# Kernel optimization log

Measured on AMD Instinct MI355X. Metric: run time of the kernel, lower is better.

The kernel has to match this reference:

```python
import jax, jax.numpy as jnp
import numpy as np

N_NODES = 50000
N_EDGES = 1600000
IN_DIM, HIDDEN, OUT_DIM = 128, 128, 64


def setup_inputs() -> dict:
    key = jax.random.key(0)
    ks = jax.random.split(key, 8)
    x = jax.random.normal(ks[0], (N_NODES, IN_DIM), dtype=jnp.float32)
    edge_index = jax.random.randint(ks[1], (2, N_EDGES), 0, N_NODES, dtype=jnp.int64)
    # SAGEConv params: lin_l applied to aggregated neighbors (with bias),
    # lin_r applied to root/self features (no bias) -- PyG defaults.
    def lin_init(k, fan_in, fan_out):
        bound = 1.0 / np.sqrt(fan_in)
        return jax.random.uniform(k, (fan_in, fan_out), jnp.float32, -bound, bound)
    W1_l = lin_init(ks[2], IN_DIM, HIDDEN)
    W1_r = lin_init(ks[3], IN_DIM, HIDDEN)
    b1 = jnp.zeros((HIDDEN,), jnp.float32)
    W2_l = lin_init(ks[4], HIDDEN, OUT_DIM)
    W2_r = lin_init(ks[5], HIDDEN, OUT_DIM)
    b2 = jnp.zeros((OUT_DIM,), jnp.float32)
    return {"x": x, "edge_index": edge_index, "W1_l": W1_l, "W1_r": W1_r,
            "b1": b1, "W2_l": W2_l, "W2_r": W2_r, "b2": b2}


def _sage_conv(h, src, dst, n_nodes, W_l, W_r, b):
    # gather messages from source nodes, mean-aggregate at destinations
    msg = h[src]                                              # [E, D]
    agg_sum = jax.ops.segment_sum(msg, dst, num_segments=n_nodes)
    deg = jax.ops.segment_sum(jnp.ones((src.shape[0],), h.dtype), dst,
                              num_segments=n_nodes)
    agg_mean = agg_sum / jnp.maximum(deg, 1.0)[:, None]       # [N, D]
    return agg_mean @ W_l + h @ W_r + b


def reference(x, edge_index, W1_l, W1_r, b1, W2_l, W2_r, b2):
    n = x.shape[0]
    src, dst = edge_index[0], edge_index[1]
    h = jax.nn.relu(_sage_conv(x, src, dst, n, W1_l, W1_r, b1))
    return _sage_conv(h, src, dst, n, W2_l, W2_r, b2)
```

## Files before the change

kernel.cpp:

```cpp
#include <hip/hip_runtime.h>

#define NN 50000
#define NE 1600000
#define BSTRIDE 96
#define BNODES 25
#define C_BKT 2000
#define P1_BLKS 256
#define P1_CHUNK 6250
#define ZID 50000
#define XCVT_BLKS 1563
#define WCVT_BLKS 48
#define PP_PREP (XCVT_BLKS + WCVT_BLKS)
#define RGRP 3128

typedef __bf16 bf16x8 __attribute__((ext_vector_type(8)));
typedef float  f32x4  __attribute__((ext_vector_type(4)));
typedef float  f32x2  __attribute__((ext_vector_type(2)));

__device__ __forceinline__ float bfLo(uint u) { union { uint i; float f; } v; v.i = u << 16; return v.f; }
__device__ __forceinline__ float bfHi(uint u) { union { uint i; float f; } v; v.i = u & 0xffff0000u; return v.f; }
__device__ __forceinline__ f32x2 bfPair(uint u) {
    union { uint i[2]; f32x2 f; } v; v.i[0] = u << 16; v.i[1] = u & 0xffff0000u; return v.f;
}
__device__ __forceinline__ ushort f2bf(float f) {
    union { float f; uint i; } v; v.f = f;
    uint r = v.i + 0x7fffu + ((v.i >> 16) & 1u);
    return (ushort)(r >> 16);
}
__device__ __forceinline__ uint pack2(float a, float b) {
    return (uint)f2bf(a) | ((uint)f2bf(b) << 16);
}
__device__ __forceinline__ bf16x8 load8(const ushort* p) {
    union { uint4 u; bf16x8 b; } v; v.u = *(const uint4*)p; return v.b;
}

#define ACC8P(u) { b0 += bfPair(u.x); b1 += bfPair(u.y); b2 += bfPair(u.z); b3 += bfPair(u.w); }

#define CVA(u, o) { f32x2 p0 = __builtin_amdgcn_cvt_pk_f32_fp8((int)(u), 0); \
                    f32x2 p1 = __builtin_amdgcn_cvt_pk_f32_fp8((int)(u), 1); \
                    a[(o)] += p0; a[(o)+1] += p1; }
#define ACCF8(v) { CVA((v).x, 0); CVA((v).y, 2); CVA((v).z, 4); CVA((v).w, 6); }

__device__ __forceinline__ int pkOff(int n, int k) {
    return (((n >> 4) * 4 + (k >> 5)) * 512) + (((k >> 3) & 3) * 128) + ((n & 15) * 8) + (k & 7);
}

__global__ __launch_bounds__(1024) void k_pp(
    const float4* __restrict__ x, ushort* __restrict__ xbp, uint* __restrict__ xf8,
    const float* __restrict__ W1l, const float* __restrict__ W1r,
    const float* __restrict__ W2l, const float* __restrict__ W2r,
    ushort* __restrict__ T1l, ushort* __restrict__ T1r,
    ushort* __restrict__ T2l, ushort* __restrict__ T2r,
    const int* __restrict__ src, const int* __restrict__ dst,
    uint* __restrict__ cells, uint* __restrict__ offc, ushort* __restrict__ hW) {
    __shared__ uint hist[C_BKT + 1];
    __shared__ uint part[250];
    const int b = blockIdx.x;
    const int tid = threadIdx.x;
    if (b < XCVT_BLKS) {
        int i = b * 1024 + tid;
        if (i < NN * 128 / 4) {
            float4 v = x[i];
            int r = i >> 5, k0 = (i & 31) * 4;
            ushort4 o; o.x = f2bf(v.x); o.y = f2bf(v.y); o.z = f2bf(v.z); o.w = f2bf(v.w);
            *(ushort4*)(xbp + pkOff(r, k0)) = o;
            uint rr = (uint)__builtin_amdgcn_cvt_pk_fp8_f32(v.x, v.y, 0, 0);
            rr = (uint)__builtin_amdgcn_cvt_pk_fp8_f32(v.z, v.w, (int)rr, 1);
            xf8[i] = rr;
        } else if (b == XCVT_BLKS - 1) {
            if (tid >= 512 && tid < 544) xf8[(size_t)ZID * 32 + (tid - 512)] = 0;
            else if (tid >= 544 && tid < 576) ((uint*)hW)[(size_t)ZID * 32 + (tid - 544)] = 0;
        }
    } else if (b < PP_PREP) {
        int i = (b - XCVT_BLKS) * 1024 + tid;
        if (i < 16384) {
            int k = i >> 7, n = i & 127; T1l[pkOff(n, k)] = f2bf(W1l[i]);
        } else if (i < 32768) {
            int j = i - 16384; int k = j >> 7, n = j & 127; T1r[pkOff(n, k)] = f2bf(W1r[j]);
        } else if (i < 40960) {
            int j = i - 32768; int k = j >> 6, n = j & 63;  T2l[pkOff(n, k)] = f2bf(W2l[j]);
        } else {
            int j = i - 40960; int k = j >> 6, n = j & 63;  T2r[pkOff(n, k)] = f2bf(W2r[j]);
        }
    } else {
        const int b2 = b - PP_PREP;
        for (int i = tid; i < C_BKT; i += 1024) hist[i] = 0;
        __syncthreads();
        const int beg = b2 * P1_CHUNK;
        for (int i = beg + tid; i < beg + P1_CHUNK; i += 1024)
            atomicAdd(&hist[dst[i] / BNODES], 1);
        __syncthreads();
        if (tid < 250) {
            uint s = 0;
            #pragma unroll
            for (int k = 0; k < 8; k++) {
                uint t = hist[tid * 8 + k];
                hist[tid * 8 + k] = s;
                s += t;
            }
            part[tid] = s;
        }
        __syncthreads();
        if (tid == 0) {
            uint run = 0;
            for (int t = 0; t < 250; t++) { uint tmp = part[t]; part[t] = run; run += tmp; }
        }
        __syncthreads();
        if (tid < 250) {
            uint bs = part[tid];
            if (bs) {
                #pragma unroll
                for (int k = 0; k < 8; k++) hist[tid * 8 + k] += bs;
            }
        }
        __syncthreads();
        for (int c = tid; c < C_BKT; c += 1024) {
            uint st = hist[c];
            uint en = (c == C_BKT - 1) ? (uint)P1_CHUNK : hist[c + 1];
            offc[(size_t)c * P1_BLKS + b2] = st | ((en - st) << 16);
        }
        __syncthreads();
        uint* myCells = cells + (size_t)b2 * P1_CHUNK;
        for (int i = beg + tid; i < beg + P1_CHUNK; i += 1024) {
            int d = dst[i];
            int s = src[i];
            int c = d / BNODES;
            uint p = atomicAdd(&hist[c], 1);
            myCells[p] = ((uint)(d - c * BNODES) << 16) | (uint)s;
        }
    }
}

__global__ __launch_bounds__(256) void k_pagg(
    const uint* __restrict__ cells, const uint* __restrict__ offc,
    const uchar* __restrict__ xf8, ushort* __restrict__ col,
    int* __restrict__ deg, ushort* __restrict__ aggp) {
    __shared__ uint hist[BNODES];
    __shared__ __align__(16) ushort colS[BNODES * BSTRIDE];
    const int bid = blockIdx.x;
    const int c = (bid & 7) * 250 + (bid >> 3);
    const int tid = threadIdx.x;
    if (tid < BNODES) hist[tid] = 0;
    __syncthreads();
    {
        uint v = offc[(size_t)c * P1_BLKS + tid];
        int st = (int)(v & 0xFFFF), n = (int)(v >> 16);
        const uint* cell = cells + (size_t)tid * P1_CHUNK + st;
        for (int j = 0; j < n; j++) {
            uint e = cell[j];
            int dl = e >> 16;
            uint p = atomicAdd(&hist[dl], 1);
            if (p < BSTRIDE) colS[dl * BSTRIDE + p] = (ushort)(e & 0xFFFF);
        }
    }
    __syncthreads();
    const int nodeBase = c * BNODES;
    if (tid < BNODES) {
        deg[nodeBase + tid] = (int)hist[tid];
        int dd = min((int)hist[tid], BSTRIDE);
        int dr = (dd + 7) & ~7;
        for (int j = dd; j < dr; j++) colS[tid * BSTRIDE + j] = (ushort)ZID;
    }
    __syncthreads();
    {
        uint4* cg = (uint4*)(col + (size_t)nodeBase * BSTRIDE);
        const uint4* cs = (const uint4*)colS;
        for (int i = tid; i < BNODES * BSTRIDE / 8; i += 256) cg[i] = cs[i];
    }
    const int wave = tid >> 6, lane = tid & 63;
    const int q = lane >> 3;
    const int cc = lane & 7;
    for (int ln = wave; ln < BNODES; ln += 4) {
        int d = (int)hist[ln];
        int dd = min(d, BSTRIDE);
        int nb = ((dd + 7) & ~7) >> 3;
        const int base = ln * BSTRIDE;
        f32x2 a[8];
        #pragma unroll
        for (int i = 0; i < 8; i++) a[i] = (f32x2){0.f, 0.f};
        int t = 0;
        for (; t + 4 <= nb; t += 4) {
            int s0 = (int)colS[base + t * 8 + q];
            int s1 = (int)colS[base + t * 8 + 8 + q];
            int s2 = (int)colS[base + t * 8 + 16 + q];
            int s3 = (int)colS[base + t * 8 + 24 + q];
            uint4 u0 = *(const uint4*)(xf8 + (size_t)s0 * 128 + cc * 16);
            uint4 u1 = *(const uint4*)(xf8 + (size_t)s1 * 128 + cc * 16);
            uint4 u2 = *(const uint4*)(xf8 + (size_t)s2 * 128 + cc * 16);
            uint4 u3 = *(const uint4*)(xf8 + (size_t)s3 * 128 + cc * 16);
            ACCF8(u0); ACCF8(u1); ACCF8(u2); ACCF8(u3);
        }
        for (; t < nb; t++) {
            int s = (int)colS[base + t * 8 + q];
            uint4 u = *(const uint4*)(xf8 + (size_t)s * 128 + cc * 16);
            ACCF8(u);
        }
        #pragma unroll
        for (int m = 8; m < 64; m <<= 1) {
            #pragma unroll
            for (int i = 0; i < 8; i++) {
                f32x2 t2;
                t2.x = __shfl_xor(a[i].x, m);
                t2.y = __shfl_xor(a[i].y, m);
                a[i] += t2;
            }
        }
        if (q == 0) {
            int node = nodeBase + ln;
            float inv = 1.f / fmaxf((float)d, 1.f);
            #pragma unroll
            for (int i = 0; i < 8; i++) a[i] *= inv;
            int basep = ((node >> 4) * 4 + (cc >> 1)) * 512 + ((cc & 1) * 2) * 128 + (node & 15) * 8;
            uint4 o;
            o.x = pack2(a[0].x, a[0].y);
            o.y = pack2(a[1].x, a[1].y);
            o.z = pack2(a[2].x, a[2].y);
            o.w = pack2(a[3].x, a[3].y);
            *(uint4*)(aggp + basep) = o;
            o.x = pack2(a[4].x, a[4].y);
            o.y = pack2(a[5].x, a[5].y);
            o.z = pack2(a[6].x, a[6].y);
            o.w = pack2(a[7].x, a[7].y);
            *(uint4*)(aggp + basep + 128) = o;
        }
    }
}

#define PAD1 136
__global__ __launch_bounds__(256) void k_gemm12(
    const ushort* __restrict__ aggp, const ushort* __restrict__ xbp,
    const ushort* __restrict__ T1l, const ushort* __restrict__ T1r,
    const ushort* __restrict__ T2l, const ushort* __restrict__ T2r,
    const float* __restrict__ b1, const float* __restrict__ b2,
    ushort* __restrict__ hW, float* __restrict__ outp) {
    __shared__ ushort hS[2][16 * PAD1];
    const int lane = threadIdx.x & 63;
    const int wave = threadIdx.x >> 6;
    const int s = wave >> 1;
    const int ch = wave & 1;
    const int quad = lane >> 4, r16 = lane & 15;
    const int row0 = blockIdx.x * 32 + s * 16;
    const int g = blockIdx.x * 2 + s;
    ushort* myS = &hS[s][0];

    f32x4 acc[4];
    #pragma unroll
    for (int nt = 0; nt < 4; nt++) acc[nt] = (f32x4){0.f, 0.f, 0.f, 0.f};
    #pragma unroll
    for (int kt = 0; kt < 4; kt++) {
        bf16x8 aAgg = load8(aggp + (size_t)(g * 4 + kt) * 512 + lane * 8);
        bf16x8 aXb  = load8(xbp  + (size_t)(g * 4 + kt) * 512 + lane * 8);
        #pragma unroll
        for (int nt = 0; nt < 4; nt++) {
            const int tile = ((ch * 4 + nt) * 4 + kt) * 512 + lane * 8;
            acc[nt] = __builtin_amdgcn_mfma_f32_16x16x32_bf16(aAgg, load8(T1l + tile), acc[nt], 0, 0, 0);
            acc[nt] = __builtin_amdgcn_mfma_f32_16x16x32_bf16(aXb,  load8(T1r + tile), acc[nt], 0, 0, 0);
        }
    }
    #pragma unroll
    for (int nt = 0; nt < 4; nt++) {
        int cc = ch * 64 + nt * 16 + r16;
        float bv = b1[cc];
        #pragma unroll
        for (int i = 0; i < 4; i++)
            myS[(quad * 4 + i) * PAD1 + cc] = f2bf(fmaxf(acc[nt][i] + bv, 0.f));
    }
    __syncthreads();

    f32x4 acc2[2], acc3[2];
    #pragma unroll
    for (int nt = 0; nt < 2; nt++) {
        acc2[nt] = (f32x4){0.f, 0.f, 0.f, 0.f};
        acc3[nt] = (f32x4){0.f, 0.f, 0.f, 0.f};
    }
    #pragma unroll
    for (int kt = 0; kt < 4; kt++) {
        bf16x8 ah = load8(&myS[r16 * PAD1 + kt * 32 + quad * 8]);
        #pragma unroll
        for (int nt = 0; nt < 2; nt++) {
            const int tile = ((ch * 2 + nt) * 4 + kt) * 512 + lane * 8;
            acc2[nt] = __builtin_amdgcn_mfma_f32_16x16x32_bf16(ah, load8(T2l + tile), acc2[nt], 0, 0, 0);
            acc3[nt] = __builtin_amdgcn_mfma_f32_16x16x32_bf16(ah, load8(T2r + tile), acc3[nt], 0, 0, 0);
        }
    }
    #pragma unroll
    for (int nt = 0; nt < 2; nt++) {
        int cc = ch * 32 + nt * 16 + r16;
        float bv = b2[cc];
        #pragma unroll
        for (int i = 0; i < 4; i++) {
            int rr = row0 + quad * 4 + i;
            if (rr < NN) {
                hW[(size_t)rr * 64 + cc] = f2bf(acc2[nt][i]);
                outp[(size_t)rr * 64 + cc] = acc3[nt][i] + bv;
            }
        }
    }
}

__global__ __launch_bounds__(256) void k_agg64f(
    const ushort* __restrict__ hW, const ushort* __restrict__ col,
    const int* __restrict__ deg, const float* __restrict__ outp,
    float* __restrict__ out) {
    __shared__ __align__(16) ushort colB[4 * BSTRIDE];
    const int tid = threadIdx.x;
    const int node0 = blockIdx.x * 4;
    if (tid < 48) {
        const uint4* cg = (const uint4*)(col + (size_t)node0 * BSTRIDE);
        *(uint4*)&colB[tid * 8] = cg[tid];
    }
    __syncthreads();
    const int wave = tid >> 6, lane = tid & 63;
    const int node = node0 + wave;
    const int q = lane >> 3;
    const int c = lane & 7;
    const int base = wave * BSTRIDE;
    int d = deg[node];
    int dd = min(d, BSTRIDE);
    int nb = ((dd + 7) & ~7) >> 3;
    f32x2 b0 = {0.f,0.f}, b1 = {0.f,0.f}, b2 = {0.f,0.f}, b3 = {0.f,0.f};
    int t = 0;
    for (; t + 4 <= nb; t += 4) {
        int s0 = (int)colB[base + t * 8 + q];
        int s1 = (int)colB[base + t * 8 + 8 + q];
        int s2 = (int)colB[base + t * 8 + 16 + q];
        int s3 = (int)colB[base + t * 8 + 24 + q];
        uint4 u0 = *(const uint4*)(hW + (size_t)s0 * 64 + c * 8);
        uint4 u1 = *(const uint4*)(hW + (size_t)s1 * 64 + c * 8);
        uint4 u2 = *(const uint4*)(hW + (size_t)s2 * 64 + c * 8);
        uint4 u3 = *(const uint4*)(hW + (size_t)s3 * 64 + c * 8);
        ACC8P(u0); ACC8P(u1); ACC8P(u2); ACC8P(u3);
    }
    for (; t < nb; t++) {
        int s = (int)colB[base + t * 8 + q];
        uint4 u = *(const uint4*)(hW + (size_t)s * 64 + c * 8);
        ACC8P(u);
    }
    #pragma unroll
    for (int m = 8; m < 64; m <<= 1) {
        f32x2 t0, t1, t2, t3;
        t0.x = __shfl_xor(b0.x, m); t0.y = __shfl_xor(b0.y, m);
        t1.x = __shfl_xor(b1.x, m); t1.y = __shfl_xor(b1.y, m);
        t2.x = __shfl_xor(b2.x, m); t2.y = __shfl_xor(b2.y, m);
        t3.x = __shfl_xor(b3.x, m); t3.y = __shfl_xor(b3.y, m);
        b0 += t0; b1 += t1; b2 += t2; b3 += t3;
    }
    if (q == 0) {
        float inv = 1.f / fmaxf((float)d, 1.f);
        float4 p0 = *(const float4*)(outp + (size_t)node * 64 + c * 8);
        float4 p1 = *(const float4*)(outp + (size_t)node * 64 + c * 8 + 4);
        float4 o;
        o.x = b0.x * inv + p0.x; o.y = b0.y * inv + p0.y;
        o.z = b1.x * inv + p0.z; o.w = b1.y * inv + p0.w;
        *(float4*)(out + (size_t)node * 64 + c * 8) = o;
        o.x = b2.x * inv + p1.x; o.y = b2.y * inv + p1.y;
        o.z = b3.x * inv + p1.z; o.w = b3.y * inv + p1.w;
        *(float4*)(out + (size_t)node * 64 + c * 8 + 4) = o;
    }
}

extern "C" void kernel_launch(void* const* d_in, const int* in_sizes, int n_in,
                              void* d_out, int out_size, void* d_ws, size_t ws_size,
                              hipStream_t stream) {
    const float* x   = (const float*)d_in[0];
    const int*   ei  = (const int*)d_in[1];
    const float* W1l = (const float*)d_in[2];
    const float* W1r = (const float*)d_in[3];
    const float* b1  = (const float*)d_in[4];
    const float* W2l = (const float*)d_in[5];
    const float* W2r = (const float*)d_in[6];
    const float* b2  = (const float*)d_in[7];
    float* out = (float*)d_out;

    const int* src = ei;
    const int* dst = ei + NE;

    char* w = (char*)d_ws;
    ushort* col   = (ushort*)w;                  w += (size_t)NN * BSTRIDE * 2;
    int* deg      = (int*)w;                     w += (size_t)50048 * 4;
    uint* offc    = (uint*)w;                    w += (size_t)C_BKT * P1_BLKS * 4;
    ushort* xbp   = (ushort*)w;                  w += (size_t)RGRP * 2048 * 2;
    ushort* T1l   = (ushort*)w;                  w += 128 * 128 * 2;
    ushort* T1r   = (ushort*)w;                  w += 128 * 128 * 2;
    ushort* T2l   = (ushort*)w;                  w += 64 * 128 * 2;
    ushort* T2r   = (ushort*)w;                  w += 64 * 128 * 2;
    ushort* aggp  = (ushort*)w;                  w += (size_t)RGRP * 2048 * 2;
    ushort* hW    = (ushort*)w;                  w += (size_t)(NN + 16) * 64 * 2;
    float* outp   = (float*)w;                   w += (size_t)NN * 64 * 4;
    uchar* xf8    = (uchar*)w;                   w += (size_t)(NN + 16) * 128;
    uint* cells   = (uint*)w;                    w += (size_t)NE * 4;

    k_pp<<<PP_PREP + P1_BLKS, 1024, 0, stream>>>(
        (const float4*)x, xbp, (uint*)xf8, W1l, W1r, W2l, W2r,
        T1l, T1r, T2l, T2r, src, dst, cells, offc, hW);

    k_pagg<<<C_BKT, 256, 0, stream>>>(cells, offc, xf8, col, deg, aggp);

    k_gemm12<<<(NN + 31) / 32, 256, 0, stream>>>(aggp, xbp, T1l, T1r, T2l, T2r, b1, b2, hW, outp);

    k_agg64f<<<NN / 4, 256, 0, stream>>>(hW, col, deg, outp, out);
}
```

Before: 201.9 us.

## Fuse layer-1 aggregation with GEMM kernel using 32-node buckets

Bucket size changes from 25 to 32 nodes so each aggregation block covers exactly one 32-row GEMM tile. The aggregation and the dual-layer GEMM then run in one kernel, with the mean-aggregated features kept in shared memory instead of a global aggp buffer. This removes a kernel launch and a global write/read round trip. Padding with ZID entries is replaced by a masked remainder gather, and the bucket division becomes a shift. The cost is more shared memory per block, which lowers occupancy. The block interleave remap used for the aggregation is also dropped.

```diff
diff --git a/kernel.cpp b/kernel.cpp
--- a/kernel.cpp
+++ b/kernel.cpp
@@ -3,8 +3,8 @@
 #define NN 50000
 #define NE 1600000
 #define BSTRIDE 96
-#define BNODES 25
-#define C_BKT 2000
+#define BNODES 32
+#define C_BKT 1564
 #define P1_BLKS 256
 #define P1_CHUNK 6250
 #define ZID 50000
@@ -12,13 +12,12 @@
 #define WCVT_BLKS 48
 #define PP_PREP (XCVT_BLKS + WCVT_BLKS)
 #define RGRP 3128
+#define SCN 196
 
 typedef __bf16 bf16x8 __attribute__((ext_vector_type(8)));
 typedef float  f32x4  __attribute__((ext_vector_type(4)));
 typedef float  f32x2  __attribute__((ext_vector_type(2)));
 
-__device__ __forceinline__ float bfLo(uint u) { union { uint i; float f; } v; v.i = u << 16; return v.f; }
-__device__ __forceinline__ float bfHi(uint u) { union { uint i; float f; } v; v.i = u & 0xffff0000u; return v.f; }
 __device__ __forceinline__ f32x2 bfPair(uint u) {
     union { uint i[2]; f32x2 f; } v; v.i[0] = u << 16; v.i[1] = u & 0xffff0000u; return v.f;
 }
@@ -53,17 +52,17 @@
     ushort* __restrict__ T2l, ushort* __restrict__ T2r,
     const int* __restrict__ src, const int* __restrict__ dst,
     uint* __restrict__ cells, uint* __restrict__ offc, ushort* __restrict__ hW) {
-    __shared__ uint hist[C_BKT + 1];
-    __shared__ uint part[250];
+    __shared__ uint hist[SCN * 8 + 1];
+    __shared__ uint part[SCN];
     const int b = blockIdx.x;
     const int tid = threadIdx.x;
     if (b < XCVT_BLKS) {
         int i = b * 1024 + tid;
         if (i < NN * 128 / 4) {
             float4 v = x[i];
-            int r = i >> 5, k0 = (i & 31) * 4;
+            int r = i >> 5, j = i & 31;
             ushort4 o; o.x = f2bf(v.x); o.y = f2bf(v.y); o.z = f2bf(v.z); o.w = f2bf(v.w);
-            *(ushort4*)(xbp + pkOff(r, k0)) = o;
+            *(ushort4*)(xbp + pkOff(r, j * 4)) = o;
             uint rr = (uint)__builtin_amdgcn_cvt_pk_fp8_f32(v.x, v.y, 0, 0);
             rr = (uint)__builtin_amdgcn_cvt_pk_fp8_f32(v.z, v.w, (int)rr, 1);
             xf8[i] = rr;
@@ -84,13 +83,13 @@
         }
     } else {
         const int b2 = b - PP_PREP;
-        for (int i = tid; i < C_BKT; i += 1024) hist[i] = 0;
+        for (int i = tid; i < SCN * 8; i += 1024) hist[i] = 0;
         __syncthreads();
         const int beg = b2 * P1_CHUNK;
         for (int i = beg + tid; i < beg + P1_CHUNK; i += 1024)
-            atomicAdd(&hist[dst[i] / BNODES], 1);
-        __syncthreads();
-        if (tid < 250) {
+            atomicAdd(&hist[dst[i] >> 5], 1);
+        __syncthreads();
+        if (tid < SCN) {
             uint s = 0;
             #pragma unroll
             for (int k = 0; k < 8; k++) {
@@ -103,10 +102,10 @@
         __syncthreads();
         if (tid == 0) {
             uint run = 0;
-            for (int t = 0; t < 250; t++) { uint tmp = part[t]; part[t] = run; run += tmp; }
-        }
-        __syncthreads();
-        if (tid < 250) {
+            for (int t = 0; t < SCN; t++) { uint tmp = part[t]; part[t] = run; run += tmp; }
+        }
+        __syncthreads();
+        if (tid < SCN) {
             uint bs = part[tid];
             if (bs) {
                 #pragma unroll
@@ -124,21 +123,26 @@
         for (int i = beg + tid; i < beg + P1_CHUNK; i += 1024) {
             int d = dst[i];
             int s = src[i];
-            int c = d / BNODES;
-            uint p = atomicAdd(&hist[c], 1);
-            myCells[p] = ((uint)(d - c * BNODES) << 16) | (uint)s;
-        }
-    }
-}
-
-__global__ __launch_bounds__(256) void k_pagg(
+            uint p = atomicAdd(&hist[d >> 5], 1);
+            myCells[p] = ((uint)(d & 31) << 16) | (uint)s;
+        }
+    }
+}
+
+#define PAD1 136
+__global__ __launch_bounds__(256) void k_fuse(
     const uint* __restrict__ cells, const uint* __restrict__ offc,
-    const uchar* __restrict__ xf8, ushort* __restrict__ col,
-    int* __restrict__ deg, ushort* __restrict__ aggp) {
+    const uchar* __restrict__ xf8, const ushort* __restrict__ xbp,
+    const ushort* __restrict__ T1l, const ushort* __restrict__ T1r,
+    const ushort* __restrict__ T2l, const ushort* __restrict__ T2r,
+    const float* __restrict__ b1, const float* __restrict__ b2,
+    ushort* __restrict__ col, int* __restrict__ deg,
+    ushort* __restrict__ hW, float* __restrict__ outp) {
     __shared__ uint hist[BNODES];
     __shared__ __align__(16) ushort colS[BNODES * BSTRIDE];
-    const int bid = blockIdx.x;
-    const int c = (bid & 7) * 250 + (bid >> 3);
+    __shared__ __align__(16) ushort aggS[2 * 4 * 512];
+    __shared__ ushort hS[2][16 * PAD1];
+    const int c = blockIdx.x;
     const int tid = threadIdx.x;
     if (tid < BNODES) hist[tid] = 0;
     __syncthreads();
@@ -155,13 +159,7 @@
     }
     __syncthreads();
     const int nodeBase = c * BNODES;
-    if (tid < BNODES) {
-        deg[nodeBase + tid] = (int)hist[tid];
-        int dd = min((int)hist[tid], BSTRIDE);
-        int dr = (dd + 7) & ~7;
-        for (int j = dd; j < dr; j++) colS[tid * BSTRIDE + j] = (ushort)ZID;
-    }
-    __syncthreads();
+    if (tid < BNODES) deg[nodeBase + tid] = (int)hist[tid];
     {
         uint4* cg = (uint4*)(col + (size_t)nodeBase * BSTRIDE);
         const uint4* cs = (const uint4*)colS;
@@ -173,13 +171,14 @@
     for (int ln = wave; ln < BNODES; ln += 4) {
         int d = (int)hist[ln];
         int dd = min(d, BSTRIDE);
-        int nb = ((dd + 7) & ~7) >> 3;
+        int nf = dd >> 3;
+        int rem = dd & 7;
         const int base = ln * BSTRIDE;
         f32x2 a[8];
         #pragma unroll
         for (int i = 0; i < 8; i++) a[i] = (f32x2){0.f, 0.f};
         int t = 0;
-        for (; t + 4 <= nb; t += 4) {
+        for (; t + 4 <= nf; t += 4) {
             int s0 = (int)colS[base + t * 8 + q];
             int s1 = (int)colS[base + t * 8 + 8 + q];
             int s2 = (int)colS[base + t * 8 + 16 + q];
@@ -190,8 +189,14 @@
             uint4 u3 = *(const uint4*)(xf8 + (size_t)s3 * 128 + cc * 16);
             ACCF8(u0); ACCF8(u1); ACCF8(u2); ACCF8(u3);
         }
-        for (; t < nb; t++) {
+        for (; t < nf; t++) {
             int s = (int)colS[base + t * 8 + q];
+            uint4 u = *(const uint4*)(xf8 + (size_t)s * 128 + cc * 16);
+            ACCF8(u);
+        }
+        if (rem) {
+            int slot = nf * 8 + q;
+            int s = (slot < dd) ? (int)colS[base + slot] : ZID;
             uint4 u = *(const uint4*)(xf8 + (size_t)s * 128 + cc * 16);
             ACCF8(u);
         }
@@ -206,41 +211,29 @@
             }
         }
         if (q == 0) {
-            int node = nodeBase + ln;
             float inv = 1.f / fmaxf((float)d, 1.f);
             #pragma unroll
             for (int i = 0; i < 8; i++) a[i] *= inv;
-            int basep = ((node >> 4) * 4 + (cc >> 1)) * 512 + ((cc & 1) * 2) * 128 + (node & 15) * 8;
+            int off = (ln >> 4) * 2048 + (cc >> 1) * 512 + ((cc & 1) * 2) * 128 + (ln & 15) * 8;
             uint4 o;
             o.x = pack2(a[0].x, a[0].y);
             o.y = pack2(a[1].x, a[1].y);
             o.z = pack2(a[2].x, a[2].y);
             o.w = pack2(a[3].x, a[3].y);
-            *(uint4*)(aggp + basep) = o;
+            *(uint4*)(aggS + off) = o;
             o.x = pack2(a[4].x, a[4].y);
             o.y = pack2(a[5].x, a[5].y);
             o.z = pack2(a[6].x, a[6].y);
             o.w = pack2(a[7].x, a[7].y);
-            *(uint4*)(aggp + basep + 128) = o;
-        }
-    }
-}
-
-#define PAD1 136
-__global__ __launch_bounds__(256) void k_gemm12(
-    const ushort* __restrict__ aggp, const ushort* __restrict__ xbp,
-    const ushort* __restrict__ T1l, const ushort* __restrict__ T1r,
-    const ushort* __restrict__ T2l, const ushort* __restrict__ T2r,
-    const float* __restrict__ b1, const float* __restrict__ b2,
-    ushort* __restrict__ hW, float* __restrict__ outp) {
-    __shared__ ushort hS[2][16 * PAD1];
-    const int lane = threadIdx.x & 63;
-    const int wave = threadIdx.x >> 6;
+            *(uint4*)(aggS + off + 128) = o;
+        }
+    }
+    __syncthreads();
     const int s = wave >> 1;
     const int ch = wave & 1;
     const int quad = lane >> 4, r16 = lane & 15;
-    const int row0 = blockIdx.x * 32 + s * 16;
-    const int g = blockIdx.x * 2 + s;
+    const int row0 = c * 32 + s * 16;
+    const int g = c * 2 + s;
     ushort* myS = &hS[s][0];
 
     f32x4 acc[4];
@@ -248,7 +241,7 @@
     for (int nt = 0; nt < 4; nt++) acc[nt] = (f32x4){0.f, 0.f, 0.f, 0.f};
     #pragma unroll
     for (int kt = 0; kt < 4; kt++) {
-        bf16x8 aAgg = load8(aggp + (size_t)(g * 4 + kt) * 512 + lane * 8);
+        bf16x8 aAgg = load8(aggS + s * 2048 + kt * 512 + lane * 8);
         bf16x8 aXb  = load8(xbp  + (size_t)(g * 4 + kt) * 512 + lane * 8);
         #pragma unroll
         for (int nt = 0; nt < 4; nt++) {
@@ -259,11 +252,11 @@
     }
     #pragma unroll
     for (int nt = 0; nt < 4; nt++) {
-        int cc = ch * 64 + nt * 16 + r16;
-        float bv = b1[cc];
+        int cx = ch * 64 + nt * 16 + r16;
+        float bv = b1[cx];
         #pragma unroll
         for (int i = 0; i < 4; i++)
-            myS[(quad * 4 + i) * PAD1 + cc] = f2bf(fmaxf(acc[nt][i] + bv, 0.f));
+            myS[(quad * 4 + i) * PAD1 + cx] = f2bf(fmaxf(acc[nt][i] + bv, 0.f));
     }
     __syncthreads();
 
@@ -285,14 +278,14 @@
     }
     #pragma unroll
     for (int nt = 0; nt < 2; nt++) {
-        int cc = ch * 32 + nt * 16 + r16;
-        float bv = b2[cc];
+        int cx = ch * 32 + nt * 16 + r16;
+        float bv = b2[cx];
         #pragma unroll
         for (int i = 0; i < 4; i++) {
             int rr = row0 + quad * 4 + i;
             if (rr < NN) {
-                hW[(size_t)rr * 64 + cc] = f2bf(acc2[nt][i]);
-                outp[(size_t)rr * 64 + cc] = acc3[nt][i] + bv;
+                hW[(size_t)rr * 64 + cx] = f2bf(acc2[nt][i]);
+                outp[(size_t)rr * 64 + cx] = acc3[nt][i] + bv;
             }
         }
     }
@@ -317,10 +310,11 @@
     const int base = wave * BSTRIDE;
     int d = deg[node];
     int dd = min(d, BSTRIDE);
-    int nb = ((dd + 7) & ~7) >> 3;
+    int nf = dd >> 3;
+    int rem = dd & 7;
     f32x2 b0 = {0.f,0.f}, b1 = {0.f,0.f}, b2 = {0.f,0.f}, b3 = {0.f,0.f};
     int t = 0;
-    for (; t + 4 <= nb; t += 4) {
+    for (; t + 4 <= nf; t += 4) {
         int s0 = (int)colB[base + t * 8 + q];
         int s1 = (int)colB[base + t * 8 + 8 + q];
         int s2 = (int)colB[base + t * 8 + 16 + q];
@@ -331,8 +325,14 @@
         uint4 u3 = *(const uint4*)(hW + (size_t)s3 * 64 + c * 8);
         ACC8P(u0); ACC8P(u1); ACC8P(u2); ACC8P(u3);
     }
-    for (; t < nb; t++) {
+    for (; t < nf; t++) {
         int s = (int)colB[base + t * 8 + q];
+        uint4 u = *(const uint4*)(hW + (size_t)s * 64 + c * 8);
+        ACC8P(u);
+    }
+    if (rem) {
+        int slot = nf * 8 + q;
+        int s = (slot < dd) ? (int)colB[base + slot] : ZID;
         uint4 u = *(const uint4*)(hW + (size_t)s * 64 + c * 8);
         ACC8P(u);
     }
@@ -376,7 +376,7 @@
     const int* dst = ei + NE;
 
     char* w = (char*)d_ws;
-    ushort* col   = (ushort*)w;                  w += (size_t)NN * BSTRIDE * 2;
+    ushort* col   = (ushort*)w;                  w += (size_t)50048 * BSTRIDE * 2;
     int* deg      = (int*)w;                     w += (size_t)50048 * 4;
     uint* offc    = (uint*)w;                    w += (size_t)C_BKT * P1_BLKS * 4;
     ushort* xbp   = (ushort*)w;                  w += (size_t)RGRP * 2048 * 2;
@@ -384,7 +384,6 @@
     ushort* T1r   = (ushort*)w;                  w += 128 * 128 * 2;
     ushort* T2l   = (ushort*)w;                  w += 64 * 128 * 2;
     ushort* T2r   = (ushort*)w;                  w += 64 * 128 * 2;
-    ushort* aggp  = (ushort*)w;                  w += (size_t)RGRP * 2048 * 2;
     ushort* hW    = (ushort*)w;                  w += (size_t)(NN + 16) * 64 * 2;
     float* outp   = (float*)w;                   w += (size_t)NN * 64 * 4;
     uchar* xf8    = (uchar*)w;                   w += (size_t)(NN + 16) * 128;
@@ -394,9 +393,8 @@
         (const float4*)x, xbp, (uint*)xf8, W1l, W1r, W2l, W2r,
         T1l, T1r, T2l, T2r, src, dst, cells, offc, hW);
 
-    k_pagg<<<C_BKT, 256, 0, stream>>>(cells, offc, xf8, col, deg, aggp);
-
-    k_gemm12<<<(NN + 31) / 32, 256, 0, stream>>>(aggp, xbp, T1l, T1r, T2l, T2r, b1, b2, hW, outp);
+    k_fuse<<<C_BKT, 256, 0, stream>>>(cells, offc, xf8, xbp,
+        T1l, T1r, T2l, T2r, b1, b2, col, deg, hW, outp);
 
     k_agg64f<<<NN / 4, 256, 0, stream>>>(hW, col, deg, outp, out);
 }
```

Measured after the change: 212.4 us. 1.05x slower.
